# Optimization experiments

Measured on AMD Instinct MI355X. Metric: run time of the kernel, lower is better.

## Reference

```python
import jax, jax.numpy as jnp
import numpy as np

B, M, N, I, O, NM = 16, 256, 256, 64, 64, 16


def setup_inputs() -> dict:
    key = jax.random.key(0)
    k1, k2, k3, k4, k5 = jax.random.split(key, 5)
    glorot = 1.0 / np.sqrt(I + O)
    return {
        "x": jax.random.normal(k1, (B, M, N, I), dtype=jnp.float32),
        "fw1": jax.random.normal(k2, (I, O, NM, NM, 2), dtype=jnp.float32) * glorot,
        "fw2": jax.random.normal(k3, (I, O, NM, NM, 2), dtype=jnp.float32) * glorot,
        "W": jax.random.normal(k4, (I, O), dtype=jnp.float32) * glorot,
        "b": jnp.zeros((O,), dtype=jnp.float32),
    }


def reference(x, fw1, fw2, W, b):
    # x: [B, M, N, I] -> [B, I, M, N]
    Bs, Ms, Ns, Is = x.shape
    nm = fw1.shape[2]
    xt = jnp.transpose(x, (0, 3, 1, 2))
    # forward rFFT over spatial dims, scaled by 1/sqrt(M*N) as in the TF code
    x_ft = jnp.fft.rfft2(xt, s=(Ms, Ns))  # [B, I, M, N//2+1] complex64
    x_ft = x_ft / jnp.asarray(np.sqrt(Ms * Ns), dtype=x_ft.dtype)
    # complex weights (stack-of-2 real/imag -> complex); complex einsum is
    # exactly the real/imag stacked matmul in the original
    w1 = jax.lax.complex(fw1[..., 0], fw1[..., 1])
    w2 = jax.lax.complex(fw2[..., 0], fw2[..., 1])
    top = jnp.einsum('bixy,ioxy->boxy', x_ft[:, :, :nm, :nm], w1)
    bot = jnp.einsum('bixy,ioxy->boxy', x_ft[:, :, -nm:, :nm], w2)
    mid = jnp.zeros((Bs, top.shape[1], Ms - 2 * nm, nm), dtype=top.dtype)
    out_ft = jnp.concatenate([top, mid, bot], axis=2)          # [B, O, M, nm]
    pad = jnp.zeros((Bs, top.shape[1], Ms, Ms // 2 + 1 - nm), dtype=top.dtype)
    out_ft = jnp.concatenate([out_ft, pad], axis=3)            # [B, O, M, M//2+1]
    y = jnp.fft.irfft2(out_ft, s=(Ns, Ms))                     # [B, O, N, M]
    # TF rescale: sqrt(prod of last two dims of out_ft) = sqrt(N*(M//2+1))
    y = y * jnp.asarray(np.sqrt(Ns * (Ms // 2 + 1)), dtype=y.dtype)
    y = jnp.transpose(y, (0, 2, 3, 1))                         # [B, M, N, O]
    return jax.nn.relu(y @ W + b + y)
```

## Files before the change

### kernel.cpp

```cpp
#include <hip/hip_runtime.h>
#include <hip/hip_bf16.h>


#define PI2F 6.283185307179586f

typedef __attribute__((ext_vector_type(8))) short short8v;
typedef __attribute__((ext_vector_type(4))) float f32x4;

static __device__ __forceinline__ unsigned short f_to_bf16(float f) {
  unsigned int u = __float_as_uint(f);
  u += 0x7fffu + ((u >> 16) & 1u);
  return (unsigned short)(u >> 16);
}
static __device__ __forceinline__ unsigned int pack_bf16(float lo, float hi) {
  return (unsigned int)f_to_bf16(lo) | ((unsigned int)f_to_bf16(hi) << 16);
}

__global__ __launch_bounds__(256) void k_prep(const float* __restrict__ fw1,
                                              const float* __restrict__ fw2,
                                              unsigned int* __restrict__ wTb,
                                              unsigned short* __restrict__ Eg,
                                              unsigned short* __restrict__ CSg,
                                              const float* __restrict__ Wg,
                                              unsigned short* __restrict__ Wtb) {
  int t = threadIdx.x;
  if (blockIdx.x == 256) {
    const float SC = 1.0f / 256.0f;
#pragma unroll
    for (int ky = 0; ky < 16; ++ky) {
      int idx = (ky * t) & 255;
      float ss, cc;
      sincosf(PI2F * (float)idx * (1.0f / 256.0f), &ss, &cc);
      Eg[(2 * ky) * 256 + t]     = f_to_bf16(cc * SC);
      Eg[(2 * ky + 1) * 256 + t] = f_to_bf16(-ss * SC);
      CSg[t * 32 + 2 * ky]       = f_to_bf16(cc);
      CSg[t * 32 + 2 * ky + 1]   = f_to_bf16(ss);
    }
#pragma unroll
    for (int k = 0; k < 16; ++k) {
      int p = k * 256 + t;
      Wtb[(p & 63) * 64 + (p >> 6)] = f_to_bf16(Wg[p]);
    }
    return;
  }
  int a  = blockIdx.x >> 3;
  int ic = blockIdx.x & 7;
  const float* w = (a < 16) ? fw1 : fw2;
  int xx = a & 15;
#pragma unroll
  for (int k = 0; k < 2; ++k) {
    int p = k * 256 + t;
    int i = ic * 8 + (p >> 6);
    int o = p & 63;
    const float4* s4 = reinterpret_cast<const float4*>(
        w + ((((size_t)i * 64 + o) * 16 + xx) * 16) * 2);
#pragma unroll
    for (int j = 0; j < 8; ++j) {
      float4 q = s4[j];
      wTb[(((size_t)(2 * j) * 32 + a) * 64 + i) * 64 + o]     = pack_bf16(q.x, q.y);
      wTb[(((size_t)(2 * j + 1) * 32 + a) * 64 + i) * 64 + o] = pack_bf16(q.z, q.w);
    }
  }
}

__global__ __launch_bounds__(256) void k1_mfma(const float* __restrict__ x,
                                               const unsigned short* __restrict__ Eg,
                                               unsigned int* __restrict__ Tb) {
  __shared__ __align__(16) unsigned short El[32 * 264];
  __shared__ __align__(16) float xs[2][2048];
  int bm = blockIdx.x;
  int b = bm >> 8, m = bm & 255;
  int tid = threadIdx.x;

  {
    const unsigned int* src = reinterpret_cast<const unsigned int*>(Eg);
    unsigned int* dst = reinterpret_cast<unsigned int*>(El);
#pragma unroll
    for (int t = 0; t < 16; ++t) {
      int idx = t * 256 + tid;
      dst[(idx >> 7) * 132 + (idx & 127)] = src[idx];
    }
  }

  const float* xrow = x + (size_t)bm * 16384;
  int lane = tid & 63, w = tid >> 6;
  int r16 = lane & 15, g4 = lane >> 4;

  int r0 = tid >> 4;
  int c4 = (tid & 15) * 4;
  int off0 = r0 * 64 + (c4 ^ (((r0 >> 3) & 3) << 4));
  int r1 = 16 + r0;
  int off1 = r1 * 64 + (c4 ^ (((r1 >> 3) & 3) << 4));
  int colr = (w * 16 + r16) ^ (g4 << 4);

  {
    const float4* s = reinterpret_cast<const float4*>(xrow);
    float4 v0 = s[tid], v1 = s[256 + tid];
    *reinterpret_cast<float4*>(&xs[0][off0]) = v0;
    *reinterpret_cast<float4*>(&xs[0][off1]) = v1;
  }
  __syncthreads();

  f32x4 z = {0.f, 0.f, 0.f, 0.f};
  f32x4 acc0 = z, acc1 = z;

#pragma unroll
  for (int c = 0; c < 8; ++c) {
    int cur = c & 1;
    if (c < 7) {
      const float4* s = reinterpret_cast<const float4*>(xrow + (c + 1) * 2048);
      float4 v0 = s[tid], v1 = s[256 + tid];
      *reinterpret_cast<float4*>(&xs[cur ^ 1][off0]) = v0;
      *reinterpret_cast<float4*>(&xs[cur ^ 1][off1]) = v1;
    }
    const float* xb = &xs[cur][g4 * 8 * 64 + colr];
    float xv[8];
#pragma unroll
    for (int j = 0; j < 8; ++j) xv[j] = xb[j * 64];
    short8v bfr;
#pragma unroll
    for (int j = 0; j < 8; ++j) bfr[j] = (short)f_to_bf16(xv[j]);
    int nb = c * 32 + g4 * 8;
    short8v a0 = *reinterpret_cast<const short8v*>(&El[r16 * 264 + nb]);
    short8v a1 = *reinterpret_cast<const short8v*>(&El[(16 + r16) * 264 + nb]);
    acc0 = __builtin_amdgcn_mfma_f32_16x16x32_bf16(a0, bfr, acc0, 0, 0, 0);
    acc1 = __builtin_amdgcn_mfma_f32_16x16x32_bf16(a1, bfr, acc1, 0, 0, 0);
    __syncthreads();
  }

  int i = w * 16 + r16;
#pragma unroll
  for (int mt = 0; mt < 2; ++mt) {
    f32x4 av = (mt == 0) ? acc0 : acc1;
    int ky_a = mt * 8 + g4 * 2;
    Tb[((size_t)(b * 16 + ky_a) * 256 + m) * 64 + i]     = pack_bf16(av[0], av[1]);
    Tb[((size_t)(b * 16 + ky_a + 1) * 256 + m) * 64 + i] = pack_bf16(av[2], av[3]);
  }
}

__global__ __launch_bounds__(1024) void k23g(const unsigned int* __restrict__ Tb,
                                             const unsigned int* __restrict__ wTb,
                                             unsigned int* __restrict__ Gb) {
  __shared__ float Xpr[4][2048];
  __shared__ float Xpi[4][2048];
  __shared__ float ct[256], st[256];
  int bky = blockIdx.x;
  int ky = bky & 15;
  int tid = threadIdx.x;

  if (tid < 256) {
    float ssv, ccv;
    sincosf(PI2F * (float)tid * (1.0f / 256.0f), &ssv, &ccv);
    ct[tid] = ccv;
    st[tid] = ssv;
  }

  int mc = tid >> 8, ih = tid & 15, ag = (tid >> 4) & 15;
  int m0 = mc * 64;
  const uint4* Tp4 = reinterpret_cast<const uint4*>(Tb) + (size_t)bky * 4096 + ih;

  float cd1, sd1n, cd2, sd2n;
  { float ss, cc; sincosf(PI2F * (float)ag * (1.0f / 256.0f), &ss, &cc); cd1 = cc; sd1n = -ss; }
  { float ss, cc; sincosf(PI2F * (float)(ag - 16) * (1.0f / 256.0f), &ss, &cc); cd2 = cc; sd2n = -ss; }
  float c1, s1, c2, s2;
  { int t = (ag * m0) & 255; float ss, cc; sincosf(PI2F * (float)t * (1.0f / 256.0f), &ss, &cc); c1 = cc; s1 = -ss; }
  { int t = ((ag + 240) * m0) & 255; float ss, cc; sincosf(PI2F * (float)t * (1.0f / 256.0f), &ss, &cc); c2 = cc; s2 = -ss; }

  float xr1[4], xi1[4], xr2[4], xi2[4];
#pragma unroll
  for (int ii = 0; ii < 4; ++ii) { xr1[ii] = xi1[ii] = xr2[ii] = xi2[ii] = 0.0f; }

#pragma unroll 4
  for (int m = 0; m < 64; ++m) {
    uint4 q = Tp4[(size_t)(m0 + m) * 16];
    unsigned int dv[4] = {q.x, q.y, q.z, q.w};
    float tre[4], tim[4];
#pragma unroll
    for (int ii = 0; ii < 4; ++ii) {
      tre[ii] = __uint_as_float(dv[ii] << 16);
      tim[ii] = __uint_as_float(dv[ii] & 0xffff0000u);
    }
#pragma unroll
    for (int ii = 0; ii < 4; ++ii) {
      xr1[ii] += tre[ii] * c1 - tim[ii] * s1;
      xi1[ii] += tre[ii] * s1 + tim[ii] * c1;
      xr2[ii] += tre[ii] * c2 - tim[ii] * s2;
      xi2[ii] += tre[ii] * s2 + tim[ii] * c2;
    }
    float cn;
    cn = c1 * cd1 - s1 * sd1n; s1 = c1 * sd1n + s1 * cd1; c1 = cn;
    cn = c2 * cd2 - s2 * sd2n; s2 = c2 * sd2n + s2 * cd2; c2 = cn;
  }
#pragma unroll
  for (int ii = 0; ii < 4; ++ii) {
    Xpr[mc][ag * 64 + ih * 4 + ii]        = xr1[ii];
    Xpi[mc][ag * 64 + ih * 4 + ii]        = xi1[ii];
    Xpr[mc][(ag + 16) * 64 + ih * 4 + ii] = xr2[ii];
    Xpi[mc][(ag + 16) * 64 + ih * 4 + ii] = xi2[ii];
  }
  __syncthreads();

  float red_r[2], red_i[2];
#pragma unroll
  for (int j = 0; j < 2; ++j) {
    int s = j * 1024 + tid;
    red_r[j] = Xpr[0][s] + Xpr[1][s] + Xpr[2][s] + Xpr[3][s];
    red_i[j] = Xpi[0][s] + Xpi[1][s] + Xpi[2][s] + Xpi[3][s];
  }
  __syncthreads();
#pragma unroll
  for (int j = 0; j < 2; ++j) {
    int s = j * 1024 + tid;
    Xpr[0][s] = red_r[j];
    Xpi[0][s] = red_i[j];
  }
  __syncthreads();

  int o = tid & 63, ab = tid >> 6;
#pragma unroll
  for (int half = 0; half < 2; ++half) {
    int a = ab + half * 16;
    const unsigned int* wp = wTb + (size_t)(ky * 32 + a) * 4096 + o;
    float ore = 0.0f, oim = 0.0f;
    for (int i = 0; i < 64; ++i) {
      float xr = Xpr[0][a * 64 + i];
      float xi = Xpi[0][a * 64 + i];
      unsigned int wv = wp[i * 64];
      float wr = __uint_as_float(wv << 16);
      float wi = __uint_as_float(wv & 0xffff0000u);
      ore += xr * wr - xi * wi;
      oim += xr * wi + xi * wr;
    }
    Xpr[1][a * 64 + o] = ore;
    Xpi[1][a * 64 + o] = oim;
  }
  __syncthreads();

  {
    const float sc = 0.002772904280510622f * ((ky == 0) ? 1.0f : 2.0f);
    unsigned int* Gp = Gb + (size_t)bky * 16384 + o;
#pragma unroll 2
    for (int j = 0; j < 16; ++j) {
      int u = ab * 16 + j;
      float accr = 0.0f, acci = 0.0f;
#pragma unroll 8
      for (int a = 0; a < 32; ++a) {
        int kx = (a < 16) ? a : (224 + a);
        int t = (kx * u) & 255;
        float cv = ct[t], sv = st[t];
        float ofr = Xpr[1][a * 64 + o];
        float ofi = Xpi[1][a * 64 + o];
        accr += ofr * cv - ofi * sv;
        acci += ofr * sv + ofi * cv;
      }
      Gp[(size_t)u * 64] = pack_bf16(accr * sc, -acci * sc);
    }
  }
}

__global__ __launch_bounds__(256) void k5_mfma(const unsigned int* __restrict__ Gb,
                                               const unsigned short* __restrict__ CSg,
                                               const unsigned short* __restrict__ Wtb,
                                               const float* __restrict__ bias,
                                               float* __restrict__ out) {
  __shared__ __align__(16) unsigned short yl[256 * 72];

  int blk = blockIdx.x;
  int tid = threadIdx.x;
  int lane = tid & 63, w = tid >> 6;
  int r16 = lane & 15, g4 = lane >> 4;
  int kc0 = g4 * 8;

  f32x4 z = {0.f, 0.f, 0.f, 0.f};
  f32x4 acc[4][4];

  int b = blk >> 8, u = blk & 255;
  const unsigned int* Gp = Gb + (size_t)b * 262144 + (size_t)u * 64;
  short8v af[4], bfx[4];
#pragma unroll
  for (int vt = 0; vt < 4; ++vt)
    af[vt] = *reinterpret_cast<const short8v*>(&CSg[(w * 64 + vt * 16 + r16) * 32 + kc0]);
#pragma unroll
  for (int ot = 0; ot < 4; ++ot) {
    union { short8v s; unsigned int d[4]; } bu;
#pragma unroll
    for (int q = 0; q < 4; ++q)
      bu.d[q] = Gp[(size_t)(g4 * 4 + q) * 16384 + ot * 16 + r16];
    bfx[ot] = bu.s;
  }
#pragma unroll
  for (int vt = 0; vt < 4; ++vt)
#pragma unroll
    for (int ot = 0; ot < 4; ++ot)
      acc[vt][ot] = __builtin_amdgcn_mfma_f32_16x16x32_bf16(af[vt], bfx[ot], z, 0, 0, 0);

#pragma unroll
  for (int vt = 0; vt < 4; ++vt)
#pragma unroll
    for (int ot = 0; ot < 4; ++ot)
#pragma unroll
      for (int r = 0; r < 4; ++r)
        yl[(w * 64 + vt * 16 + g4 * 4 + r) * 72 + ot * 16 + r16] = f_to_bf16(acc[vt][ot][r]);

#pragma unroll
  for (int ot = 0; ot < 4; ++ot) {
    float bv = bias[ot * 16 + r16];
#pragma unroll
    for (int vt = 0; vt < 4; ++vt)
#pragma unroll
      for (int r = 0; r < 4; ++r) acc[vt][ot][r] += bv;
  }

#pragma unroll
  for (int ks = 0; ks < 2; ++ks) {
    int k0 = ks * 32 + kc0;
    short8v ya[4], wb[4];
#pragma unroll
    for (int vt = 0; vt < 4; ++vt)
      ya[vt] = *reinterpret_cast<const short8v*>(&yl[(w * 64 + vt * 16 + r16) * 72 + k0]);
#pragma unroll
    for (int ot = 0; ot < 4; ++ot)
      wb[ot] = *reinterpret_cast<const short8v*>(&Wtb[(ot * 16 + r16) * 64 + k0]);
#pragma unroll
    for (int vt = 0; vt < 4; ++vt)
#pragma unroll
      for (int ot = 0; ot < 4; ++ot)
        acc[vt][ot] = __builtin_amdgcn_mfma_f32_16x16x32_bf16(ya[vt], wb[ot], acc[vt][ot], 0, 0, 0);
  }

  float* ob = out + (size_t)blk * 16384;
  float* tw = reinterpret_cast<float*>(&yl[w * 4608]);
#pragma unroll
  for (int vt = 0; vt < 4; ++vt) {
#pragma unroll
    for (int ot = 0; ot < 4; ++ot)
#pragma unroll
      for (int r = 0; r < 4; ++r)
        tw[(g4 * 4 + r) * 68 + ot * 16 + r16] = fmaxf(acc[vt][ot][r], 0.0f);
    float* obase = ob + (size_t)(w * 64 + vt * 16) * 64;
#pragma unroll
    for (int q = 0; q < 4; ++q) {
      float4 vv = *reinterpret_cast<const float4*>(
          &tw[(q * 4 + (lane >> 4)) * 68 + (lane & 15) * 4]);
      *reinterpret_cast<float4*>(&obase[q * 256 + lane * 4]) = vv;
    }
  }
}

extern "C" void kernel_launch(void* const* d_in, const int* in_sizes, int n_in,
                              void* d_out, int out_size, void* d_ws, size_t ws_size,
                              hipStream_t stream) {
  const float* x   = (const float*)d_in[0];
  const float* fw1 = (const float*)d_in[1];
  const float* fw2 = (const float*)d_in[2];
  const float* W   = (const float*)d_in[3];
  const float* bb  = (const float*)d_in[4];
  float* out = (float*)d_out;

  float* ws = (float*)d_ws;
  unsigned int* wTb  = (unsigned int*)ws;
  unsigned int* Tb   = (unsigned int*)(ws + 2097152);
  unsigned int* Gb   = (unsigned int*)(ws + 6291456);
  unsigned short* Eg  = (unsigned short*)(ws + 10485760);
  unsigned short* CSg = Eg + 8192;
  unsigned short* Wtb = CSg + 8192;

  hipLaunchKernelGGL(k_prep,   dim3(257),  dim3(256),  0, stream,
                     fw1, fw2, wTb, Eg, CSg, W, Wtb);
  hipLaunchKernelGGL(k1_mfma,  dim3(4096), dim3(256),  0, stream, x, Eg, Tb);
  hipLaunchKernelGGL(k23g,     dim3(256),  dim3(1024), 0, stream, Tb, wTb, Gb);
  hipLaunchKernelGGL(k5_mfma,  dim3(4096), dim3(256),  0, stream,
                     Gb, CSg, Wtb, bb, out);
}
```

Before: 228.0 us.

## Move inverse kx DFT from mixing kernel into output MFMA kernel

The partial inverse DFT along kx (32 modes to 256 rows) is removed from the spectral mixing kernel, which now writes the compact mixed spectrum OF (fp32 complex, 32 modes per ky) instead of the expanded bf16 G buffer. Each output block recomputes its own row u of G from OF in shared memory before the MFMA stage. This shrinks the intermediate buffer and its global write/read traffic, and spreads the DFT work across 4096 blocks instead of 256 large ones. In exchange, each output block rereads its batch's OF slice (about 256KB per batch, shared by 256 blocks through cache) and pays for extra sincos table setup and a shared-memory sync. The partial-sum reduction in the mixing kernel is also made in place, dropping one barrier.

After: 235.3 us. 3.2% more time.

```diff
diff --git a/kernel.cpp b/kernel.cpp
--- a/kernel.cpp
+++ b/kernel.cpp
@@ -138,22 +138,14 @@
   }
 }
 
-__global__ __launch_bounds__(1024) void k23g(const unsigned int* __restrict__ Tb,
-                                             const unsigned int* __restrict__ wTb,
-                                             unsigned int* __restrict__ Gb) {
+__global__ __launch_bounds__(1024) void k23_mix(const unsigned int* __restrict__ Tb,
+                                                const unsigned int* __restrict__ wTb,
+                                                float* __restrict__ OF) {
   __shared__ float Xpr[4][2048];
   __shared__ float Xpi[4][2048];
-  __shared__ float ct[256], st[256];
   int bky = blockIdx.x;
   int ky = bky & 15;
   int tid = threadIdx.x;
-
-  if (tid < 256) {
-    float ssv, ccv;
-    sincosf(PI2F * (float)tid * (1.0f / 256.0f), &ssv, &ccv);
-    ct[tid] = ccv;
-    st[tid] = ssv;
-  }
 
   int mc = tid >> 8, ih = tid & 15, ag = (tid >> 4) & 15;
   int m0 = mc * 64;
@@ -200,19 +192,11 @@
   }
   __syncthreads();
 
-  float red_r[2], red_i[2];
 #pragma unroll
   for (int j = 0; j < 2; ++j) {
     int s = j * 1024 + tid;
-    red_r[j] = Xpr[0][s] + Xpr[1][s] + Xpr[2][s] + Xpr[3][s];
-    red_i[j] = Xpi[0][s] + Xpi[1][s] + Xpi[2][s] + Xpi[3][s];
-  }
-  __syncthreads();
-#pragma unroll
-  for (int j = 0; j < 2; ++j) {
-    int s = j * 1024 + tid;
-    Xpr[0][s] = red_r[j];
-    Xpi[0][s] = red_i[j];
+    Xpr[0][s] += Xpr[1][s] + Xpr[2][s] + Xpr[3][s];
+    Xpi[0][s] += Xpi[1][s] + Xpi[2][s] + Xpi[3][s];
   }
   __syncthreads();
 
@@ -231,42 +215,62 @@
       ore += xr * wr - xi * wi;
       oim += xr * wi + xi * wr;
     }
-    Xpr[1][a * 64 + o] = ore;
-    Xpi[1][a * 64 + o] = oim;
-  }
-  __syncthreads();
-
-  {
-    const float sc = 0.002772904280510622f * ((ky == 0) ? 1.0f : 2.0f);
-    unsigned int* Gp = Gb + (size_t)bky * 16384 + o;
-#pragma unroll 2
-    for (int j = 0; j < 16; ++j) {
-      int u = ab * 16 + j;
-      float accr = 0.0f, acci = 0.0f;
-#pragma unroll 8
-      for (int a = 0; a < 32; ++a) {
-        int kx = (a < 16) ? a : (224 + a);
-        int t = (kx * u) & 255;
-        float cv = ct[t], sv = st[t];
-        float ofr = Xpr[1][a * 64 + o];
-        float ofi = Xpi[1][a * 64 + o];
-        accr += ofr * cv - ofi * sv;
-        acci += ofr * sv + ofi * cv;
-      }
-      Gp[(size_t)u * 64] = pack_bf16(accr * sc, -acci * sc);
-    }
-  }
-}
-
-__global__ __launch_bounds__(256) void k5_mfma(const unsigned int* __restrict__ Gb,
+    reinterpret_cast<float2*>(OF)[((size_t)bky * 32 + a) * 64 + o] =
+        make_float2(ore, oim);
+  }
+}
+
+__global__ __launch_bounds__(256) void k5_mfma(const float* __restrict__ OF,
                                                const unsigned short* __restrict__ CSg,
                                                const unsigned short* __restrict__ Wtb,
                                                const float* __restrict__ bias,
                                                float* __restrict__ out) {
   __shared__ __align__(16) unsigned short yl[256 * 72];
+  __shared__ __align__(16) unsigned short gl[64 * 40];
+  __shared__ float ct[256], st[256];
 
   int blk = blockIdx.x;
+  int b = blk >> 8, u = blk & 255;
   int tid = threadIdx.x;
+  {
+    float ssv, ccv;
+    sincosf(PI2F * (float)tid * (1.0f / 256.0f), &ssv, &ccv);
+    ct[tid] = ccv;
+    st[tid] = ssv;
+  }
+  __syncthreads();
+
+  {
+    int o = tid & 63, kcg = tid >> 6;
+    const float2* OFb = reinterpret_cast<const float2*>(OF) + (size_t)b * 32768;
+    float accr[4], acci[4];
+#pragma unroll
+    for (int kk = 0; kk < 4; ++kk) { accr[kk] = 0.0f; acci[kk] = 0.0f; }
+    for (int a = 0; a < 32; ++a) {
+      int kx = (a < 16) ? a : (224 + a);
+      int t = (kx * u) & 255;
+      float cv = ct[t], sv = st[t];
+#pragma unroll
+      for (int kk = 0; kk < 4; ++kk) {
+        int ky = kcg * 4 + kk;
+        float2 v = OFb[(ky * 32 + a) * 64 + o];
+        accr[kk] += v.x * cv - v.y * sv;
+        acci[kk] += v.x * sv + v.y * cv;
+      }
+    }
+    const float SC2 = 0.002772904280510622f;
+    unsigned int pk[4];
+#pragma unroll
+    for (int kk = 0; kk < 4; ++kk) {
+      int ky = kcg * 4 + kk;
+      float sc = SC2 * ((ky == 0) ? 1.0f : 2.0f);
+      pk[kk] = pack_bf16(accr[kk] * sc, -acci[kk] * sc);
+    }
+    uint4 q; q.x = pk[0]; q.y = pk[1]; q.z = pk[2]; q.w = pk[3];
+    *reinterpret_cast<uint4*>(&gl[o * 40 + kcg * 8]) = q;
+  }
+  __syncthreads();
+
   int lane = tid & 63, w = tid >> 6;
   int r16 = lane & 15, g4 = lane >> 4;
   int kc0 = g4 * 8;
@@ -274,20 +278,13 @@
   f32x4 z = {0.f, 0.f, 0.f, 0.f};
   f32x4 acc[4][4];
 
-  int b = blk >> 8, u = blk & 255;
-  const unsigned int* Gp = Gb + (size_t)b * 262144 + (size_t)u * 64;
   short8v af[4], bfx[4];
 #pragma unroll
   for (int vt = 0; vt < 4; ++vt)
     af[vt] = *reinterpret_cast<const short8v*>(&CSg[(w * 64 + vt * 16 + r16) * 32 + kc0]);
 #pragma unroll
-  for (int ot = 0; ot < 4; ++ot) {
-    union { short8v s; unsigned int d[4]; } bu;
-#pragma unroll
-    for (int q = 0; q < 4; ++q)
-      bu.d[q] = Gp[(size_t)(g4 * 4 + q) * 16384 + ot * 16 + r16];
-    bfx[ot] = bu.s;
-  }
+  for (int ot = 0; ot < 4; ++ot)
+    bfx[ot] = *reinterpret_cast<const short8v*>(&gl[(ot * 16 + r16) * 40 + kc0]);
 #pragma unroll
   for (int vt = 0; vt < 4; ++vt)
 #pragma unroll
@@ -360,15 +357,15 @@
   float* ws = (float*)d_ws;
   unsigned int* wTb  = (unsigned int*)ws;
   unsigned int* Tb   = (unsigned int*)(ws + 2097152);
-  unsigned int* Gb   = (unsigned int*)(ws + 6291456);
-  unsigned short* Eg  = (unsigned short*)(ws + 10485760);
+  float* OF          = ws + 6291456;
+  unsigned short* Eg  = (unsigned short*)(ws + 7340032);
   unsigned short* CSg = Eg + 8192;
   unsigned short* Wtb = CSg + 8192;
 
   hipLaunchKernelGGL(k_prep,   dim3(257),  dim3(256),  0, stream,
                      fw1, fw2, wTb, Eg, CSg, W, Wtb);
   hipLaunchKernelGGL(k1_mfma,  dim3(4096), dim3(256),  0, stream, x, Eg, Tb);
-  hipLaunchKernelGGL(k23g,     dim3(256),  dim3(1024), 0, stream, Tb, wTb, Gb);
+  hipLaunchKernelGGL(k23_mix,  dim3(256),  dim3(1024), 0, stream, Tb, wTb, OF);
   hipLaunchKernelGGL(k5_mfma,  dim3(4096), dim3(256),  0, stream,
-                     Gb, CSg, Wtb, bb, out);
-}
+                     OF, CSg, Wtb, bb, out);
+}
```
